# Performance work log

Hardware: AMD Instinct MI355X
Metric: run time of the kernel (lower is better)

## Reference

```python
import jax, jax.numpy as jnp
import numpy as np

HID, H, D = 128, 4, 32
NB, NP, NC = 60000, 2000, 4000
EM, EP, EI = 150000, 300000, 150000


def segment_softmax(logits, seg, n):
    # logits: [E, H], seg: [E] destination ids
    m = jax.ops.segment_max(logits, seg, num_segments=n)
    m = jnp.where(jnp.isfinite(m), m, 0.0)  # guard empty segments
    e = jnp.exp(logits - m[seg])
    s = jax.ops.segment_sum(e, seg, num_segments=n)
    return e / (s[seg] + 1e-16)


def layer_norm(x, g, b):
    mu = x.mean(-1, keepdims=True)
    v = ((x - mu) ** 2).mean(-1, keepdims=True)
    return (x - mu) / jnp.sqrt(v + 1e-5) * g + b


def setup_inputs():
    key = jax.random.key(0)
    ks = jax.random.split(key, 40)
    i = iter(range(40))
    nrm = lambda shape, s=1.0: jax.random.normal(ks[next(i)], shape, jnp.float32) * s
    w = lambda shape: nrm(shape, 0.05)
    inp = {
        'x_ball': nrm((NB, HID)),
        'x_player': nrm((NP, HID)),
        'x_context': nrm((NC, HID)),
        'em': jnp.stack([jax.random.randint(ks[next(i)], (EM,), 0, NP),
                         jax.random.randint(ks[next(i)], (EM,), 0, NB)]),
        'ep': jnp.stack([jax.random.randint(ks[next(i)], (EP,), 0, NB),
                         jax.random.randint(ks[next(i)], (EP,), 0, NB)]),
        'ei': jnp.stack([jax.random.randint(ks[next(i)], (EI,), 0, NB),
                         jax.random.randint(ks[next(i)], (EI,), 0, NC)]),
        'ea_p': nrm((EP, 1)),
        # GATv2Conv (player -matchup-> ball)
        'g_Wl': w((HID, HID)), 'g_Wr': w((HID, HID)), 'g_att': w((H, D)), 'g_b': jnp.zeros((HID,), jnp.float32),
        # TransformerConv (ball -recent_precedes-> ball), edge_dim=1
        't_Wq': w((HID, HID)), 't_bq': jnp.zeros((HID,), jnp.float32),
        't_Wk': w((HID, HID)), 't_bk': jnp.zeros((HID,), jnp.float32),
        't_Wv': w((HID, HID)), 't_bv': jnp.zeros((HID,), jnp.float32),
        't_We': w((1, HID)),
        't_Wskip': w((HID, HID)), 't_bskip': jnp.zeros((HID,), jnp.float32),
        # SAGEConv mean (ball -informs-> context)
        's_Wl': w((HID, HID)), 's_bl': jnp.zeros((HID,), jnp.float32), 's_Wr': w((HID, HID)),
        # per-type LayerNorms (only applied to types produced by the conv)
        'ln_ball_g': jnp.ones((HID,), jnp.float32), 'ln_ball_b': jnp.zeros((HID,), jnp.float32),
        'ln_ctx_g': jnp.ones((HID,), jnp.float32), 'ln_ctx_b': jnp.zeros((HID,), jnp.float32),
    }
    return inp


def reference(x_ball, x_player, x_context, em, ep, ei, ea_p,
              g_Wl, g_Wr, g_att, g_b,
              t_Wq, t_bq, t_Wk, t_bk, t_Wv, t_bv, t_We, t_Wskip, t_bskip,
              s_Wl, s_bl, s_Wr,
              ln_ball_g, ln_ball_b, ln_ctx_g, ln_ctx_b):
    # ---- GATv2Conv: player -> ball ----
    src, dst = em[0], em[1]
    xl = (x_player @ g_Wl).reshape(NP, H, D)   # src transform
    xr = (x_ball @ g_Wr).reshape(NB, H, D)     # dst transform
    e = xl[src] + xr[dst]                      # [EM, H, D]
    e = jnp.where(e > 0, e, 0.2 * e)           # leaky_relu(0.2)
    logit = jnp.einsum('ehd,hd->eh', e, g_att)
    alpha = segment_softmax(logit, dst, NB)
    gat = jax.ops.segment_sum(xl[src] * alpha[..., None], dst, num_segments=NB)
    gat = gat.reshape(NB, HID) + g_b

    # ---- TransformerConv: ball -> ball, edge_dim=1 ----
    src, dst = ep[0], ep[1]
    q = (x_ball @ t_Wq + t_bq).reshape(NB, H, D)
    k = (x_ball @ t_Wk + t_bk).reshape(NB, H, D)
    v = (x_ball @ t_Wv + t_bv).reshape(NB, H, D)
    ee = (ea_p @ t_We).reshape(EP, H, D)       # lin_edge (no bias)
    kj = k[src] + ee
    logit = jnp.einsum('ehd,ehd->eh', q[dst], kj) / jnp.sqrt(jnp.float32(D))
    alpha = segment_softmax(logit, dst, NB)
    tr = jax.ops.segment_sum((v[src] + ee) * alpha[..., None], dst, num_segments=NB)
    tr = tr.reshape(NB, HID) + x_ball @ t_Wskip + t_bskip  # root/skip connection

    # ---- SAGEConv mean: ball -> context ----
    src, dst = ei[0], ei[1]
    summ = jax.ops.segment_sum(x_ball[src], dst, num_segments=NC)
    cnt = jax.ops.segment_sum(jnp.ones((EI,), jnp.float32), dst, num_segments=NC)
    mean = summ / jnp.maximum(cnt, 1.0)[:, None]
    sage = mean @ s_Wl + s_bl + x_context @ s_Wr

    # ---- HeteroConv aggr='sum' + residual + per-type LayerNorm ----
    ball_out = layer_norm(gat + tr + x_ball, ln_ball_g, ln_ball_b)
    ctx_out = layer_norm(sage + x_context, ln_ctx_g, ln_ctx_b)
    # 'player' receives no messages -> passed through unchanged
    return (ball_out, ctx_out, x_player)
```

## Files before the change

kernel.cpp:

```cpp
#include <hip/hip_runtime.h>
#include <hip/hip_bf16.h>

#define NB 60000
#define NP 2000
#define NC 4000
#define EM_N 150000
#define EP_N 300000
#define EI_N 150000
#define POOL_N (EM_N + EP_N + EI_N)
#define SEG_TOT (NB + NB + NC)
#define SCAN_BLK 1024
#define NPART ((SEG_TOT + SCAN_BLK - 1) / SCAN_BLK)
#define BALL_TILES ((NB + 63) / 64)
#define PLYR_TILES ((NP + 63) / 64)
#define CTX_TILES ((NC + 63) / 64)
#define GEMM_BLKS (6 * BALL_TILES + PLYR_TILES + CTX_TILES)
#define FILL_BLKS ((POOL_N + 255) / 256)
#define CONVB ((NB * 16 + 255) / 256)
#define CONVC ((NC * 16 + 255) / 256)
#define CONVP ((NP * 16 + 255) / 256)
#define PREP_BLKS (NPART + 512 + CONVB + CONVC + CONVP)
#define BBALL ((NB + 3) / 4)

#define QSCALE (0.17677669529663687f * 1.4426950408889634f)
#define LOG2E 1.4426950408889634f

typedef __hip_bfloat16 bf16;
typedef unsigned int u32;
typedef __attribute__((ext_vector_type(8))) short s8v;
typedef __attribute__((ext_vector_type(4))) float f4v;

__device__ __forceinline__ short f2bs(float f) {
    bf16 h = __float2bfloat16(f);
    return __builtin_bit_cast(short, h);
}
__device__ __forceinline__ float bsToF(short s) {
    return __builtin_bit_cast(float, ((unsigned)(unsigned short)s) << 16);
}
__device__ __forceinline__ float loF(u32 v) { return bsToF((short)(v & 0xffff)); }
__device__ __forceinline__ float hiF(u32 v) { return bsToF((short)(v >> 16)); }
__device__ __forceinline__ u32 packbf(float a, float b) {
    return (u32)(unsigned short)f2bs(a) | ((u32)(unsigned short)f2bs(b) << 16);
}
__device__ __forceinline__ void gl_lds16(const void* g, void* l) {
    __builtin_amdgcn_global_load_lds((const __attribute__((address_space(1))) void*)g,
                                     (__attribute__((address_space(3))) void*)l, 16, 0, 0);
}

__global__ void hist_kernel(const int* __restrict__ em, const int* __restrict__ ep,
                            const int* __restrict__ ei, int* __restrict__ counts,
                            int* __restrict__ ranks) {
    int t = blockIdx.x * 256 + threadIdx.x;
    if (t < EM_N) ranks[t] = atomicAdd(&counts[em[EM_N + t]], 1);
    else if (t < EM_N + EP_N) ranks[t] = atomicAdd(&counts[NB + ep[EP_N + (t - EM_N)]], 1);
    else if (t < POOL_N) ranks[t] = atomicAdd(&counts[2 * NB + ei[EI_N + (t - EM_N - EP_N)]], 1);
}

__global__ void prepscan_kernel(const int* __restrict__ counts, int* __restrict__ offsets,
                                int* __restrict__ gbase,
                                const float* __restrict__ W0, const float* __restrict__ W1,
                                const float* __restrict__ W2, const float* __restrict__ W3,
                                const float* __restrict__ W4, const float* __restrict__ W5,
                                const float* __restrict__ W6, const float* __restrict__ W7,
                                ushort* __restrict__ Wt,
                                const float* __restrict__ x_ball, const float* __restrict__ x_context,
                                const float* __restrict__ x_player,
                                u32* __restrict__ xbB, u32* __restrict__ xbC, u32* __restrict__ xbP,
                                float* __restrict__ out) {
    __shared__ int sd[256];
    __shared__ int sbase;
    if (blockIdx.x < NPART) {
        int b = blockIdx.x, tid = threadIdx.x;
        int base = b * SCAN_BLK + tid * 4;
        int v[4]; int ts = 0;
#pragma unroll
        for (int j = 0; j < 4; j++) { int idx = base + j; v[j] = (idx < SEG_TOT) ? counts[idx] : 0; ts += v[j]; }
        sd[tid] = ts;
        for (int off = 1; off < 256; off <<= 1) {
            __syncthreads(); int t = (tid >= off) ? sd[tid - off] : 0;
            __syncthreads(); sd[tid] += t;
        }
        __syncthreads();
        if (tid == 255) sbase = atomicAdd(gbase, sd[255]);
        __syncthreads();
        int run = sd[tid] - ts + sbase;
#pragma unroll
        for (int j = 0; j < 4; j++) {
            int idx = base + j;
            if (idx < SEG_TOT) offsets[idx] = run;
            run += v[j];
        }
        return;
    }
    int b2 = blockIdx.x - NPART;
    if (b2 < 512) {
        int t = b2 * 256 + threadIdx.x;
        int w = t >> 14, r = t & 16383, k = r >> 7, n = r & 127;
        const float* W = (w == 0) ? W0 : (w == 1) ? W1 : (w == 2) ? W2 : (w == 3) ? W3
                       : (w == 4) ? W4 : (w == 5) ? W5 : (w == 6) ? W6 : W7;
        int sc = (n >> 5) * 32 + ((n & 1) << 4) + ((n & 31) >> 1);
        Wt[w * 16384 + (k >> 3) * 1024 + sc * 8 + (k & 7)] = (unsigned short)f2bs(W[k * 128 + n]);
        return;
    }
    int b3 = b2 - 512;
    if (b3 < CONVB) {
        int idx = b3 * 256 + threadIdx.x;
        const float4* p = (const float4*)(x_ball + (size_t)idx * 8);
        float4 u = p[0], v = p[1];
        ((uint4*)xbB)[idx] = make_uint4(packbf(u.x, u.y), packbf(u.z, u.w),
                                        packbf(v.x, v.y), packbf(v.z, v.w));
    } else if (b3 < CONVB + CONVC) {
        int idx = (b3 - CONVB) * 256 + threadIdx.x;
        const float4* p = (const float4*)(x_context + (size_t)idx * 8);
        float4 u = p[0], v = p[1];
        ((uint4*)xbC)[idx] = make_uint4(packbf(u.x, u.y), packbf(u.z, u.w),
                                        packbf(v.x, v.y), packbf(v.z, v.w));
    } else {
        int idx = (b3 - CONVB - CONVC) * 256 + threadIdx.x;
        const float4* p = (const float4*)(x_player + (size_t)idx * 8);
        float4 u = p[0], v = p[1];
        ((uint4*)xbP)[idx] = make_uint4(packbf(u.x, u.y), packbf(u.z, u.w),
                                        packbf(v.x, v.y), packbf(v.z, v.w));
        float4* po = (float4*)(out + (size_t)(NB + NC) * 128 + (size_t)idx * 8);
        po[0] = u; po[1] = v;
    }
}

__global__ __launch_bounds__(256) void gemm6_fill_kernel(
    const u32* __restrict__ xbB, const u32* __restrict__ xbP, const u32* __restrict__ xbC,
    const float* __restrict__ Aball, const float* __restrict__ Actx,
    const ushort* __restrict__ Wt,
    const float* __restrict__ bq, const float* __restrict__ bk,
    const float* __restrict__ bv_, const float* __restrict__ bskip, const float* __restrict__ bl,
    u32* __restrict__ xrP, u32* __restrict__ qP, u32* __restrict__ kvP,
    u32* __restrict__ skipP, u32* __restrict__ xlP, u32* __restrict__ xwP,
    u32* __restrict__ ctxlinP,
    const int* __restrict__ em, const int* __restrict__ ep, const int* __restrict__ ei,
    const float* __restrict__ ea_p, const int* __restrict__ offsets,
    const int* __restrict__ ranks, int2* __restrict__ pool) {
    __shared__ ushort lds[16384];
    if (blockIdx.x >= GEMM_BLKS) {
        int t = (blockIdx.x - GEMM_BLKS) * 256 + threadIdx.x;
        int seg, s; float ea = 0.f;
        if (t < EM_N) { s = em[t]; seg = em[EM_N + t]; }
        else if (t < EM_N + EP_N) { int e = t - EM_N; s = ep[e]; seg = NB + ep[EP_N + e]; ea = ea_p[e]; }
        else if (t < POOL_N) { int e = t - EM_N - EP_N; s = ei[e]; seg = 2 * NB + ei[EI_N + e]; }
        else return;
        int pos = offsets[seg] + ranks[t];
        pool[pos] = make_int2(s, __float_as_int(ea));
        return;
    }
    const int tid = threadIdx.x;
    const int lane = tid & 63;
    const int wv = tid >> 6;
    const int quad = lane >> 4, l16 = lane & 15;

    int bid = blockIdx.x;
    int w, tile, M;
    const u32* A;
    if (bid < 6 * BALL_TILES) {
        int widx = bid / BALL_TILES;
        w = (widx < 5) ? widx : 6;
        tile = bid - widx * BALL_TILES; M = NB; A = xbB;
    } else if (bid < 6 * BALL_TILES + PLYR_TILES) {
        w = 5; tile = bid - 6 * BALL_TILES; M = NP; A = xbP;
    } else {
        w = 7; tile = bid - 6 * BALL_TILES - PLYR_TILES; M = NC; A = xbC;
    }
    u32* op; const float* bp = nullptr; const float* resid = nullptr; float scale = 1.f;
    int ostride = 64, ooff = 0;
    switch (w) {
        case 0: op = xrP; break;
        case 1: op = qP; bp = bq; scale = QSCALE; break;
        case 2: op = kvP; bp = bk; ostride = 128; ooff = 0; break;
        case 3: op = kvP; bp = bv_; ostride = 128; ooff = 64; break;
        case 4: op = skipP; bp = bskip; resid = Aball; break;
        case 5: op = xlP; break;
        case 6: op = xwP; break;
        default: op = ctxlinP; bp = bl; resid = Actx; break;
    }

    {
        const ushort* src = Wt + w * 16384;
#pragma unroll
        for (int p = 0; p < 8; p++)
            gl_lds16(src + (size_t)(p * 256 + tid) * 8, lds + p * 2048 + wv * 512);
    }

    s8v a[4];
    {
        int r0 = tile * 64 + wv * 16 + l16; if (r0 >= M) r0 = M - 1;
        const s8v* ap = (const s8v*)(A + (size_t)r0 * 64 + quad * 4);
#pragma unroll
        for (int kt = 0; kt < 4; kt++) a[kt] = ap[kt * 4];
    }
    float2 bias2[4];
#pragma unroll
    for (int t = 0; t < 4; t++)
        bias2[t] = bp ? ((const float2*)bp)[t * 16 + l16] : make_float2(0.f, 0.f);
    __syncthreads();

    const int mbase = tile * 64 + wv * 16;
#pragma unroll
    for (int t = 0; t < 4; t++) {
        f4v alo = {0.f, 0.f, 0.f, 0.f}, ahi = {0.f, 0.f, 0.f, 0.f};
#pragma unroll
        for (int kt = 0; kt < 4; kt++) {
            s8v blo = *(const s8v*)(lds + (kt * 4 + quad) * 1024 + (t * 32 + l16) * 8);
            s8v bhi = *(const s8v*)(lds + (kt * 4 + quad) * 1024 + (t * 32 + 16 + l16) * 8);
            alo = __builtin_amdgcn_mfma_f32_16x16x32_bf16(a[kt], blo, alo, 0, 0, 0);
            ahi = __builtin_amdgcn_mfma_f32_16x16x32_bf16(a[kt], bhi, ahi, 0, 0, 0);
        }
#pragma unroll
        for (int r = 0; r < 4; r++) {
            int row = mbase + quad * 4 + r;
            if (row < M) {
                float vlo = (alo[r] + bias2[t].x) * scale;
                float vhi = (ahi[r] + bias2[t].y) * scale;
                if (resid) {
                    float2 x2 = ((const float2*)resid)[(size_t)row * 64 + t * 16 + l16];
                    vlo += x2.x; vhi += x2.y;
                }
                op[(size_t)row * ostride + ooff + t * 16 + l16] = packbf(vlo, vhi);
            }
        }
    }
}

__device__ __forceinline__ void gat_batch(const u32 xv[4], const bool ok[4],
                                          float xr0, float xr1, float attx, float atty,
                                          float& n0, float& n1, float& deg) {
    float p[4], xa[4], xb[4];
#pragma unroll
    for (int i = 0; i < 4; i++) {
        xa[i] = loF(xv[i]); xb[i] = hiF(xv[i]);
        float u0 = xa[i] + xr0; u0 = u0 > 0.f ? u0 : 0.2f * u0;
        float u1 = xb[i] + xr1; u1 = u1 > 0.f ? u1 : 0.2f * u1;
        p[i] = u0 * attx + u1 * atty;
    }
#pragma unroll
    for (int m = 1; m <= 8; m <<= 1) {
#pragma unroll
        for (int i = 0; i < 4; i++) p[i] += __shfl_xor(p[i], m);
    }
#pragma unroll
    for (int i = 0; i < 4; i++) {
        p[i] = ok[i] ? exp2f(p[i]) : 0.f;
        n0 += p[i] * xa[i]; n1 += p[i] * xb[i]; deg += p[i];
    }
}

__device__ __forceinline__ void tr_batch(const u32 kk[4], const u32 vv[4],
                                         const float ea[4], const bool ok[4],
                                         float q0, float q1, float dw,
                                         float& sv0, float& sv1, float& spe, float& det) {
    float p[4];
#pragma unroll
    for (int i = 0; i < 4; i++) p[i] = q0 * loF(kk[i]) + q1 * hiF(kk[i]);
#pragma unroll
    for (int m = 1; m <= 8; m <<= 1) {
#pragma unroll
        for (int i = 0; i < 4; i++) p[i] += __shfl_xor(p[i], m);
    }
#pragma unroll
    for (int i = 0; i < 4; i++) {
        p[i] = ok[i] ? exp2f(p[i] + ea[i] * dw) : 0.f;
        sv0 += p[i] * loF(vv[i]); sv1 += p[i] * hiF(vv[i]);
        spe += p[i] * ea[i]; det += p[i];
    }
}

__global__ __launch_bounds__(256) void ball_sage_kernel(
    const u32* __restrict__ xlP, const u32* __restrict__ xrP, const u32* __restrict__ qP,
    const u32* __restrict__ kvP, const u32* __restrict__ skipP, const u32* __restrict__ xwP,
    const u32* __restrict__ ctxlinP,
    const float* __restrict__ g_att, const float* __restrict__ g_b, const float* __restrict__ We,
    const int* __restrict__ offsets, const int* __restrict__ counts,
    const int2* __restrict__ pool,
    const float* __restrict__ ln_g, const float* __restrict__ ln_b,
    const float* __restrict__ cg, const float* __restrict__ cb,
    float* __restrict__ out) {
    __shared__ float part[4][128];
    const int wv = threadIdx.x >> 6, l = threadIdx.x & 63;

    if (blockIdx.x >= BBALL) {
        int c = blockIdx.x - BBALL;
        int beg = offsets[2 * NB + c], cnt = counts[2 * NB + c];
        float s0 = 0.f, s1 = 0.f;
        int j = wv;
        if (j < cnt) {
            int i0 = pool[beg + j].x;
            int idx1 = (j + 4 < cnt) ? beg + j + 4 : 0;
            int i1 = pool[idx1].x;
            u32 x0 = xwP[(size_t)i0 * 64 + l];
            u32 x1 = xwP[(size_t)i1 * 64 + l];
            for (; j < cnt; j += 4) {
                int idx2 = (j + 8 < cnt) ? beg + j + 8 : 0;
                int i2 = pool[idx2].x;
                s0 += loF(x0); s1 += hiF(x0);
                x0 = x1;
                x1 = xwP[(size_t)i2 * 64 + l];
            }
        }
        part[wv][l * 2] = s0; part[wv][l * 2 + 1] = s1;
        __syncthreads();
        if (wv == 0) {
            float m = fmaxf((float)cnt, 1.f);
            u32 cl = ctxlinP[(size_t)c * 64 + l];
            float v0 = (part[0][l * 2] + part[1][l * 2] + part[2][l * 2] + part[3][l * 2]) / m + loF(cl);
            float v1 = (part[0][l * 2 + 1] + part[1][l * 2 + 1] + part[2][l * 2 + 1] + part[3][l * 2 + 1]) / m + hiF(cl);
            float s = v0 + v1;
#pragma unroll
            for (int m2 = 1; m2 <= 32; m2 <<= 1) s += __shfl_xor(s, m2);
            float mu = s * (1.f / 128.f);
            float d0 = v0 - mu, d1 = v1 - mu;
            float qv = d0 * d0 + d1 * d1;
#pragma unroll
            for (int m2 = 1; m2 <= 32; m2 <<= 1) qv += __shfl_xor(qv, m2);
            float inv = rsqrtf(qv * (1.f / 128.f) + 1e-5f);
            float2 g2 = ((const float2*)cg)[l];
            float2 b2 = ((const float2*)cb)[l];
            ((float2*)out)[(size_t)(NB + c) * 64 + l] =
                make_float2(d0 * inv * g2.x + b2.x, d1 * inv * g2.y + b2.y);
        }
        return;
    }

    const int d = blockIdx.x * 4 + wv;
    const size_t rowD = (size_t)d * 64;
    const int ds = __builtin_amdgcn_readfirstlane(d);

    u32 xr2 = xrP[rowD + l];
    u32 q2 = qP[rowD + l];
    u32 sk = skipP[rowD + l];

    const int begG = offsets[ds], cntG = counts[ds];
    const int begT = offsets[NB + ds], cntT = counts[NB + ds];
    int gS[8];
#pragma unroll
    for (int i = 0; i < 8; i++) { int idx = (i < cntG) ? begG + i : 0; gS[i] = pool[idx].x; }
    int tS[8]; float tE[8];
#pragma unroll
    for (int i = 0; i < 8; i++) {
        int idx = (i < cntT) ? begT + i : 0;
        int2 pr = pool[idx]; tS[i] = pr.x; tE[i] = __int_as_float(pr.y);
    }

    u32 gx[8];
    if (cntG > 0) {
#pragma unroll
        for (int i = 0; i < 4; i++) gx[i] = xlP[(size_t)gS[i] * 64 + l];
        if (cntG > 4) {
#pragma unroll
            for (int i = 4; i < 8; i++) gx[i] = xlP[(size_t)gS[i] * 64 + l];
        }
    }
    u32 kk[8], vv[8];
    if (cntT > 0) {
#pragma unroll
        for (int i = 0; i < 4; i++) {
            kk[i] = kvP[(size_t)tS[i] * 128 + l];
            vv[i] = kvP[(size_t)tS[i] * 128 + 64 + l];
        }
        if (cntT > 4) {
#pragma unroll
            for (int i = 4; i < 8; i++) {
                kk[i] = kvP[(size_t)tS[i] * 128 + l];
                vv[i] = kvP[(size_t)tS[i] * 128 + 64 + l];
            }
        }
    }

    float q0 = loF(q2), q1 = hiF(q2);
    float2 we = ((const float2*)We)[l];
    float dw = q0 * we.x + q1 * we.y;
#pragma unroll
    for (int m = 1; m <= 8; m <<= 1) dw += __shfl_xor(dw, m);

    float2 attv = ((const float2*)g_att)[l];
    float attx = attv.x * LOG2E, atty = attv.y * LOG2E;
    float xr0 = loF(xr2), xr1 = hiF(xr2);
    float n0 = 0.f, n1 = 0.f, deg = 0.f;
    if (cntG > 0) {
        bool ok[4];
#pragma unroll
        for (int i = 0; i < 4; i++) ok[i] = (i < cntG);
        gat_batch(&gx[0], ok, xr0, xr1, attx, atty, n0, n1, deg);
        if (cntG > 4) {
            bool ok2[4];
#pragma unroll
            for (int i = 0; i < 4; i++) ok2[i] = (4 + i < cntG);
            gat_batch(&gx[4], ok2, xr0, xr1, attx, atty, n0, n1, deg);
        }
        for (int j = 8; j < cntG; j += 4) {
            bool ok3[4]; u32 xv[4];
#pragma unroll
            for (int i = 0; i < 4; i++) {
                ok3[i] = (j + i < cntG);
                int idx = ok3[i] ? begG + j + i : 0;
                xv[i] = xlP[(size_t)pool[idx].x * 64 + l];
            }
            gat_batch(xv, ok3, xr0, xr1, attx, atty, n0, n1, deg);
        }
    }
    float gat0 = n0 / (deg + 1e-16f), gat1 = n1 / (deg + 1e-16f);

    float sv0 = 0.f, sv1 = 0.f, spe = 0.f, det = 0.f;
    if (cntT > 0) {
        bool ok[4];
#pragma unroll
        for (int i = 0; i < 4; i++) ok[i] = (i < cntT);
        tr_batch(&kk[0], &vv[0], &tE[0], ok, q0, q1, dw, sv0, sv1, spe, det);
        if (cntT > 4) {
            bool ok2[4];
#pragma unroll
            for (int i = 0; i < 4; i++) ok2[i] = (4 + i < cntT);
            tr_batch(&kk[4], &vv[4], &tE[4], ok2, q0, q1, dw, sv0, sv1, spe, det);
        }
        for (int j = 8; j < cntT; j += 4) {
            bool ok3[4]; u32 kt2[4], vt2[4]; float ea[4];
#pragma unroll
            for (int i = 0; i < 4; i++) {
                ok3[i] = (j + i < cntT);
                int idx = ok3[i] ? begT + j + i : 0;
                int2 pr = pool[idx];
                ea[i] = __int_as_float(pr.y);
                kt2[i] = kvP[(size_t)pr.x * 128 + l];
                vt2[i] = kvP[(size_t)pr.x * 128 + 64 + l];
            }
            tr_batch(kt2, vt2, ea, ok3, q0, q1, dw, sv0, sv1, spe, det);
        }
    }
    float tr0 = (sv0 + spe * we.x) / (det + 1e-16f);
    float tr1 = (sv1 + spe * we.y) / (det + 1e-16f);

    float2 gb2 = ((const float2*)g_b)[l];
    float val0 = loF(sk) + gb2.x + gat0 + tr0;
    float val1 = hiF(sk) + gb2.y + gat1 + tr1;
    float s = val0 + val1;
#pragma unroll
    for (int m = 1; m <= 32; m <<= 1) s += __shfl_xor(s, m);
    float mu = s * (1.f / 128.f);
    float d0 = val0 - mu, d1 = val1 - mu;
    float qv = d0 * d0 + d1 * d1;
#pragma unroll
    for (int m = 1; m <= 32; m <<= 1) qv += __shfl_xor(qv, m);
    float inv = rsqrtf(qv * (1.f / 128.f) + 1e-5f);
    float2 g2 = ((const float2*)ln_g)[l];
    float2 b2 = ((const float2*)ln_b)[l];
    ((float2*)out)[rowD + l] = make_float2(d0 * inv * g2.x + b2.x, d1 * inv * g2.y + b2.y);
}

extern "C" void kernel_launch(void* const* d_in, const int* in_sizes, int n_in,
                              void* d_out, int out_size, void* d_ws, size_t ws_size,
                              hipStream_t stream) {
    const float* x_ball = (const float*)d_in[0];
    const float* x_player = (const float*)d_in[1];
    const float* x_context = (const float*)d_in[2];
    const int* em = (const int*)d_in[3];
    const int* ep = (const int*)d_in[4];
    const int* ei = (const int*)d_in[5];
    const float* ea_p = (const float*)d_in[6];
    const float* g_Wl = (const float*)d_in[7];
    const float* g_Wr = (const float*)d_in[8];
    const float* g_att = (const float*)d_in[9];
    const float* g_b = (const float*)d_in[10];
    const float* t_Wq = (const float*)d_in[11];
    const float* t_bq = (const float*)d_in[12];
    const float* t_Wk = (const float*)d_in[13];
    const float* t_bk = (const float*)d_in[14];
    const float* t_Wv = (const float*)d_in[15];
    const float* t_bv = (const float*)d_in[16];
    const float* t_We = (const float*)d_in[17];
    const float* t_Wskip = (const float*)d_in[18];
    const float* t_bskip = (const float*)d_in[19];
    const float* s_Wl = (const float*)d_in[20];
    const float* s_bl = (const float*)d_in[21];
    const float* s_Wr = (const float*)d_in[22];
    const float* ln_ball_g = (const float*)d_in[23];
    const float* ln_ball_b = (const float*)d_in[24];
    const float* ln_ctx_g = (const float*)d_in[25];
    const float* ln_ctx_b = (const float*)d_in[26];
    float* out = (float*)d_out;

    float* ws = (float*)d_ws;
    size_t o = 0;
    int* counts = (int*)(ws + o);   o += SEG_TOT;
    int* gbase = (int*)(ws + o);    o += 1;
    int* offsets = (int*)(ws + o);  o += SEG_TOT;
    int* ranks = (int*)(ws + o);    o += POOL_N;
    if (o & 1) o++;
    int2* pool = (int2*)(ws + o);   o += (size_t)POOL_N * 2;
    o = (o + 3) & ~(size_t)3;
    ushort* Wt = (ushort*)(ws + o); o += (8 * 16384) / 2;
    u32* xbB = (u32*)(ws + o);      o += (size_t)NB * 64;
    u32* xbC = (u32*)(ws + o);      o += (size_t)NC * 64;
    u32* xbP = (u32*)(ws + o);      o += (size_t)NP * 64;
    u32* xlP = (u32*)(ws + o);      o += (size_t)NP * 64;
    u32* xrP = (u32*)(ws + o);      o += (size_t)NB * 64;
    u32* qP = (u32*)(ws + o);       o += (size_t)NB * 64;
    u32* skipP = (u32*)(ws + o);    o += (size_t)NB * 64;
    u32* xwP = (u32*)(ws + o);      o += (size_t)NB * 64;
    u32* ctxlinP = (u32*)(ws + o);  o += (size_t)NC * 64;
    if (o & 1) o++;
    u32* kvP = (u32*)(ws + o);      o += (size_t)NB * 128;

    dim3 blk(256);
    hipMemsetAsync(counts, 0, (SEG_TOT + 1) * sizeof(int), stream);
    hist_kernel<<<FILL_BLKS, blk, 0, stream>>>(em, ep, ei, counts, ranks);
    prepscan_kernel<<<PREP_BLKS, blk, 0, stream>>>(
        counts, offsets, gbase, g_Wr, t_Wq, t_Wk, t_Wv, t_Wskip, g_Wl, s_Wl, s_Wr, Wt,
        x_ball, x_context, x_player, xbB, xbC, xbP, out);
    gemm6_fill_kernel<<<GEMM_BLKS + FILL_BLKS, blk, 0, stream>>>(
        xbB, xbP, xbC, x_ball, x_context, Wt, t_bq, t_bk, t_bv, t_bskip, s_bl,
        xrP, qP, kvP, skipP, xlP, xwP, ctxlinP, em, ep, ei, ea_p, offsets, ranks, pool);
    ball_sage_kernel<<<BBALL + NC, blk, 0, stream>>>(
        xlP, xrP, qP, kvP, skipP, xwP, ctxlinP, g_att, g_b, t_We,
        offsets, counts, pool, ln_ball_g, ln_ball_b, ln_ctx_g, ln_ctx_b, out);
}
```

Baseline: 289.3 us.

## Split each wave into two half-waves processing alternate edges with 4-wide feature lanes

Restructures the ball aggregation so each 64-lane wave handles two edges at a time: 32 lanes cover the 128 features with 8-byte loads (4 bf16 values per lane), and the wave halves process even and odd edges. Head reductions shrink to 3 shuffle steps, and the two halves are combined by a single xor-32 shuffle at the end. The intent is wider loads and half as many serial edge iterations per destination node. In exchange each lane carries more registers, and only half the wave writes the LayerNorm output.

```diff
diff --git a/kernel.cpp b/kernel.cpp
--- a/kernel.cpp
+++ b/kernel.cpp
@@ -227,49 +227,6 @@
     }
 }
 
-__device__ __forceinline__ void gat_batch(const u32 xv[4], const bool ok[4],
-                                          float xr0, float xr1, float attx, float atty,
-                                          float& n0, float& n1, float& deg) {
-    float p[4], xa[4], xb[4];
-#pragma unroll
-    for (int i = 0; i < 4; i++) {
-        xa[i] = loF(xv[i]); xb[i] = hiF(xv[i]);
-        float u0 = xa[i] + xr0; u0 = u0 > 0.f ? u0 : 0.2f * u0;
-        float u1 = xb[i] + xr1; u1 = u1 > 0.f ? u1 : 0.2f * u1;
-        p[i] = u0 * attx + u1 * atty;
-    }
-#pragma unroll
-    for (int m = 1; m <= 8; m <<= 1) {
-#pragma unroll
-        for (int i = 0; i < 4; i++) p[i] += __shfl_xor(p[i], m);
-    }
-#pragma unroll
-    for (int i = 0; i < 4; i++) {
-        p[i] = ok[i] ? exp2f(p[i]) : 0.f;
-        n0 += p[i] * xa[i]; n1 += p[i] * xb[i]; deg += p[i];
-    }
-}
-
-__device__ __forceinline__ void tr_batch(const u32 kk[4], const u32 vv[4],
-                                         const float ea[4], const bool ok[4],
-                                         float q0, float q1, float dw,
-                                         float& sv0, float& sv1, float& spe, float& det) {
-    float p[4];
-#pragma unroll
-    for (int i = 0; i < 4; i++) p[i] = q0 * loF(kk[i]) + q1 * hiF(kk[i]);
-#pragma unroll
-    for (int m = 1; m <= 8; m <<= 1) {
-#pragma unroll
-        for (int i = 0; i < 4; i++) p[i] += __shfl_xor(p[i], m);
-    }
-#pragma unroll
-    for (int i = 0; i < 4; i++) {
-        p[i] = ok[i] ? exp2f(p[i] + ea[i] * dw) : 0.f;
-        sv0 += p[i] * loF(vv[i]); sv1 += p[i] * hiF(vv[i]);
-        spe += p[i] * ea[i]; det += p[i];
-    }
-}
-
 __global__ __launch_bounds__(256) void ball_sage_kernel(
     const u32* __restrict__ xlP, const u32* __restrict__ xrP, const u32* __restrict__ qP,
     const u32* __restrict__ kvP, const u32* __restrict__ skipP, const u32* __restrict__ xwP,
@@ -329,126 +286,168 @@
     const int d = blockIdx.x * 4 + wv;
     const size_t rowD = (size_t)d * 64;
     const int ds = __builtin_amdgcn_readfirstlane(d);
-
-    u32 xr2 = xrP[rowD + l];
-    u32 q2 = qP[rowD + l];
-    u32 sk = skipP[rowD + l];
+    const int li = l & 31, el = l >> 5;
+
+    uint2 xr4 = ((const uint2*)(xrP + rowD))[li];
+    uint2 q4 = ((const uint2*)(qP + rowD))[li];
+    uint2 sk4 = ((const uint2*)(skipP + rowD))[li];
 
     const int begG = offsets[ds], cntG = counts[ds];
     const int begT = offsets[NB + ds], cntT = counts[NB + ds];
-    int gS[8];
-#pragma unroll
-    for (int i = 0; i < 8; i++) { int idx = (i < cntG) ? begG + i : 0; gS[i] = pool[idx].x; }
-    int tS[8]; float tE[8];
-#pragma unroll
-    for (int i = 0; i < 8; i++) {
-        int idx = (i < cntT) ? begT + i : 0;
-        int2 pr = pool[idx]; tS[i] = pr.x; tE[i] = __int_as_float(pr.y);
-    }
-
-    u32 gx[8];
+
+    int sG[4]; bool okG[4];
+    int sT[4]; float eT[4]; bool okT[4];
+#pragma unroll
+    for (int i = 0; i < 4; i++) {
+        int e = 2 * i + el;
+        okG[i] = e < cntG;
+        sG[i] = (cntG > 0) ? pool[begG + (okG[i] ? e : 0)].x : 0;
+    }
+#pragma unroll
+    for (int i = 0; i < 4; i++) {
+        int e = 2 * i + el;
+        okT[i] = e < cntT;
+        int2 pr = (cntT > 0) ? pool[begT + (okT[i] ? e : 0)] : make_int2(0, 0);
+        sT[i] = pr.x; eT[i] = __int_as_float(pr.y);
+    }
+    uint2 gx[4], kk[4], vvv[4];
     if (cntG > 0) {
 #pragma unroll
-        for (int i = 0; i < 4; i++) gx[i] = xlP[(size_t)gS[i] * 64 + l];
-        if (cntG > 4) {
-#pragma unroll
-            for (int i = 4; i < 8; i++) gx[i] = xlP[(size_t)gS[i] * 64 + l];
-        }
-    }
-    u32 kk[8], vv[8];
+        for (int i = 0; i < 4; i++) gx[i] = ((const uint2*)(xlP + (size_t)sG[i] * 64))[li];
+    }
     if (cntT > 0) {
 #pragma unroll
         for (int i = 0; i < 4; i++) {
-            kk[i] = kvP[(size_t)tS[i] * 128 + l];
-            vv[i] = kvP[(size_t)tS[i] * 128 + 64 + l];
-        }
-        if (cntT > 4) {
-#pragma unroll
-            for (int i = 4; i < 8; i++) {
-                kk[i] = kvP[(size_t)tS[i] * 128 + l];
-                vv[i] = kvP[(size_t)tS[i] * 128 + 64 + l];
+            kk[i] = ((const uint2*)(kvP + (size_t)sT[i] * 128))[li];
+            vvv[i] = ((const uint2*)(kvP + (size_t)sT[i] * 128 + 64))[li];
+        }
+    }
+
+    float xrd[4] = {loF(xr4.x), hiF(xr4.x), loF(xr4.y), hiF(xr4.y)};
+    float qd[4] = {loF(q4.x), hiF(q4.x), loF(q4.y), hiF(q4.y)};
+    float4 att4 = ((const float4*)g_att)[li];
+    float at[4] = {att4.x * LOG2E, att4.y * LOG2E, att4.z * LOG2E, att4.w * LOG2E};
+    float4 we4 = ((const float4*)We)[li];
+    float wed[4] = {we4.x, we4.y, we4.z, we4.w};
+
+    float dw = qd[0] * wed[0] + qd[1] * wed[1] + qd[2] * wed[2] + qd[3] * wed[3];
+    dw += __shfl_xor(dw, 1); dw += __shfl_xor(dw, 2); dw += __shfl_xor(dw, 4);
+
+    float n[4] = {0.f, 0.f, 0.f, 0.f}, deg = 0.f;
+    auto gat8 = [&](const uint2 g[4], const bool ok[4]) {
+        float p[4], xa[4][4];
+#pragma unroll
+        for (int i = 0; i < 4; i++) {
+            xa[i][0] = loF(g[i].x); xa[i][1] = hiF(g[i].x);
+            xa[i][2] = loF(g[i].y); xa[i][3] = hiF(g[i].y);
+            float pp = 0.f;
+#pragma unroll
+            for (int dd = 0; dd < 4; dd++) {
+                float u = xa[i][dd] + xrd[dd];
+                u = u > 0.f ? u : 0.2f * u;
+                pp += u * at[dd];
             }
-        }
-    }
-
-    float q0 = loF(q2), q1 = hiF(q2);
-    float2 we = ((const float2*)We)[l];
-    float dw = q0 * we.x + q1 * we.y;
-#pragma unroll
-    for (int m = 1; m <= 8; m <<= 1) dw += __shfl_xor(dw, m);
-
-    float2 attv = ((const float2*)g_att)[l];
-    float attx = attv.x * LOG2E, atty = attv.y * LOG2E;
-    float xr0 = loF(xr2), xr1 = hiF(xr2);
-    float n0 = 0.f, n1 = 0.f, deg = 0.f;
+            p[i] = pp;
+        }
+#pragma unroll
+        for (int m = 1; m <= 4; m <<= 1) {
+#pragma unroll
+            for (int i = 0; i < 4; i++) p[i] += __shfl_xor(p[i], m);
+        }
+#pragma unroll
+        for (int i = 0; i < 4; i++) {
+            p[i] = ok[i] ? exp2f(p[i]) : 0.f;
+#pragma unroll
+            for (int dd = 0; dd < 4; dd++) n[dd] += p[i] * xa[i][dd];
+            deg += p[i];
+        }
+    };
     if (cntG > 0) {
-        bool ok[4];
-#pragma unroll
-        for (int i = 0; i < 4; i++) ok[i] = (i < cntG);
-        gat_batch(&gx[0], ok, xr0, xr1, attx, atty, n0, n1, deg);
-        if (cntG > 4) {
-            bool ok2[4];
-#pragma unroll
-            for (int i = 0; i < 4; i++) ok2[i] = (4 + i < cntG);
-            gat_batch(&gx[4], ok2, xr0, xr1, attx, atty, n0, n1, deg);
-        }
-        for (int j = 8; j < cntG; j += 4) {
-            bool ok3[4]; u32 xv[4];
+        gat8(gx, okG);
+        for (int j = 8; j < cntG; j += 8) {
+            uint2 g2[4]; bool ok2[4];
 #pragma unroll
             for (int i = 0; i < 4; i++) {
-                ok3[i] = (j + i < cntG);
-                int idx = ok3[i] ? begG + j + i : 0;
-                xv[i] = xlP[(size_t)pool[idx].x * 64 + l];
+                int e = j + 2 * i + el;
+                ok2[i] = e < cntG;
+                int s2 = pool[begG + (ok2[i] ? e : 0)].x;
+                g2[i] = ((const uint2*)(xlP + (size_t)s2 * 64))[li];
             }
-            gat_batch(xv, ok3, xr0, xr1, attx, atty, n0, n1, deg);
-        }
-    }
-    float gat0 = n0 / (deg + 1e-16f), gat1 = n1 / (deg + 1e-16f);
-
-    float sv0 = 0.f, sv1 = 0.f, spe = 0.f, det = 0.f;
+            gat8(g2, ok2);
+        }
+    }
+#pragma unroll
+    for (int dd = 0; dd < 4; dd++) n[dd] += __shfl_xor(n[dd], 32);
+    deg += __shfl_xor(deg, 32);
+    float rdeg = 1.f / (deg + 1e-16f);
+    float gatd[4] = {n[0] * rdeg, n[1] * rdeg, n[2] * rdeg, n[3] * rdeg};
+
+    float sv[4] = {0.f, 0.f, 0.f, 0.f}, spe = 0.f, det = 0.f;
+    auto tr8 = [&](const uint2 K[4], const uint2 V[4], const float ea[4], const bool ok[4]) {
+        float p[4];
+#pragma unroll
+        for (int i = 0; i < 4; i++) {
+            p[i] = qd[0] * loF(K[i].x) + qd[1] * hiF(K[i].x)
+                 + qd[2] * loF(K[i].y) + qd[3] * hiF(K[i].y);
+        }
+#pragma unroll
+        for (int m = 1; m <= 4; m <<= 1) {
+#pragma unroll
+            for (int i = 0; i < 4; i++) p[i] += __shfl_xor(p[i], m);
+        }
+#pragma unroll
+        for (int i = 0; i < 4; i++) {
+            p[i] = ok[i] ? exp2f(p[i] + ea[i] * dw) : 0.f;
+            sv[0] += p[i] * loF(V[i].x); sv[1] += p[i] * hiF(V[i].x);
+            sv[2] += p[i] * loF(V[i].y); sv[3] += p[i] * hiF(V[i].y);
+            spe += p[i] * ea[i]; det += p[i];
+        }
+    };
     if (cntT > 0) {
-        bool ok[4];
-#pragma unroll
-        for (int i = 0; i < 4; i++) ok[i] = (i < cntT);
-        tr_batch(&kk[0], &vv[0], &tE[0], ok, q0, q1, dw, sv0, sv1, spe, det);
-        if (cntT > 4) {
-            bool ok2[4];
-#pragma unroll
-            for (int i = 0; i < 4; i++) ok2[i] = (4 + i < cntT);
-            tr_batch(&kk[4], &vv[4], &tE[4], ok2, q0, q1, dw, sv0, sv1, spe, det);
-        }
-        for (int j = 8; j < cntT; j += 4) {
-            bool ok3[4]; u32 kt2[4], vt2[4]; float ea[4];
+        tr8(kk, vvv, eT, okT);
+        for (int j = 8; j < cntT; j += 8) {
+            uint2 k2[4], v2[4]; bool ok2[4]; float ea2[4];
 #pragma unroll
             for (int i = 0; i < 4; i++) {
-                ok3[i] = (j + i < cntT);
-                int idx = ok3[i] ? begT + j + i : 0;
-                int2 pr = pool[idx];
-                ea[i] = __int_as_float(pr.y);
-                kt2[i] = kvP[(size_t)pr.x * 128 + l];
-                vt2[i] = kvP[(size_t)pr.x * 128 + 64 + l];
+                int e = j + 2 * i + el;
+                ok2[i] = e < cntT;
+                int2 pr = pool[begT + (ok2[i] ? e : 0)];
+                ea2[i] = __int_as_float(pr.y);
+                k2[i] = ((const uint2*)(kvP + (size_t)pr.x * 128))[li];
+                v2[i] = ((const uint2*)(kvP + (size_t)pr.x * 128 + 64))[li];
             }
-            tr_batch(kt2, vt2, ea, ok3, q0, q1, dw, sv0, sv1, spe, det);
-        }
-    }
-    float tr0 = (sv0 + spe * we.x) / (det + 1e-16f);
-    float tr1 = (sv1 + spe * we.y) / (det + 1e-16f);
-
-    float2 gb2 = ((const float2*)g_b)[l];
-    float val0 = loF(sk) + gb2.x + gat0 + tr0;
-    float val1 = hiF(sk) + gb2.y + gat1 + tr1;
-    float s = val0 + val1;
-#pragma unroll
-    for (int m = 1; m <= 32; m <<= 1) s += __shfl_xor(s, m);
+            tr8(k2, v2, ea2, ok2);
+        }
+    }
+#pragma unroll
+    for (int dd = 0; dd < 4; dd++) sv[dd] += __shfl_xor(sv[dd], 32);
+    spe += __shfl_xor(spe, 32);
+    det += __shfl_xor(det, 32);
+    float rdet = 1.f / (det + 1e-16f);
+    float trd[4];
+#pragma unroll
+    for (int dd = 0; dd < 4; dd++) trd[dd] = (sv[dd] + spe * wed[dd]) * rdet;
+
+    float4 gb4 = ((const float4*)g_b)[li];
+    float skd[4] = {loF(sk4.x), hiF(sk4.x), loF(sk4.y), hiF(sk4.y)};
+    float val[4] = {skd[0] + gb4.x + gatd[0] + trd[0], skd[1] + gb4.y + gatd[1] + trd[1],
+                    skd[2] + gb4.z + gatd[2] + trd[2], skd[3] + gb4.w + gatd[3] + trd[3]};
+    float s = val[0] + val[1] + val[2] + val[3];
+#pragma unroll
+    for (int m = 1; m <= 16; m <<= 1) s += __shfl_xor(s, m);
     float mu = s * (1.f / 128.f);
-    float d0 = val0 - mu, d1 = val1 - mu;
-    float qv = d0 * d0 + d1 * d1;
-#pragma unroll
-    for (int m = 1; m <= 32; m <<= 1) qv += __shfl_xor(qv, m);
+    float df[4] = {val[0] - mu, val[1] - mu, val[2] - mu, val[3] - mu};
+    float qv = df[0] * df[0] + df[1] * df[1] + df[2] * df[2] + df[3] * df[3];
+#pragma unroll
+    for (int m = 1; m <= 16; m <<= 1) qv += __shfl_xor(qv, m);
     float inv = rsqrtf(qv * (1.f / 128.f) + 1e-5f);
-    float2 g2 = ((const float2*)ln_g)[l];
-    float2 b2 = ((const float2*)ln_b)[l];
-    ((float2*)out)[rowD + l] = make_float2(d0 * inv * g2.x + b2.x, d1 * inv * g2.y + b2.y);
+    float4 g4 = ((const float4*)ln_g)[li];
+    float4 b4 = ((const float4*)ln_b)[li];
+    if (el == 0) {
+        ((float4*)out)[(size_t)d * 32 + li] =
+            make_float4(df[0] * inv * g4.x + b4.x, df[1] * inv * g4.y + b4.y,
+                        df[2] * inv * g4.z + b4.z, df[3] * inv * g4.w + b4.w);
+    }
 }
 
 extern "C" void kernel_launch(void* const* d_in, const int* in_sizes, int n_in,
```

After: 336.5 us. 16.3% more time.
